# Kernel tuning notes

Measured on AMD Instinct MI355X. Metric: run time of the kernel, lower is better.

## Reference

```python
import math
import jax, jax.numpy as jnp
import numpy as np

DIM = 192
HEADS = 4
OUT_DIM = 192

def _conv(x, w, groups=1, pad=0):
    return jax.lax.conv_general_dilated(
        x, w, window_strides=(1, 1), padding=[(pad, pad), (pad, pad)],
        feature_group_count=groups, dimension_numbers=('NCHW', 'OIHW', 'NCHW'))

def setup_inputs() -> dict:
    key = jax.random.key(0)
    ks = jax.random.split(key, 8)
    b, c, h, w = 8, DIM, 128, 128
    x = jax.random.normal(ks[0], (b, c, h, w), dtype=jnp.float32)
    y = jax.random.normal(ks[1], (b, c, h, w), dtype=jnp.float32)
    s = 0.02
    kv_w = jax.random.normal(ks[2], (2 * DIM, DIM, 1, 1), dtype=jnp.float32) * s
    kv_dw_w = jax.random.normal(ks[3], (2 * DIM, 1, 3, 3), dtype=jnp.float32) * s  # depthwise, groups=2*dim
    q_w = jax.random.normal(ks[4], (DIM, DIM, 1, 1), dtype=jnp.float32) * s
    q_dw_w = jax.random.normal(ks[5], (DIM, DIM, 3, 3), dtype=jnp.float32) * s  # dense 3x3 (groups=1 in source)
    proj_w = jax.random.normal(ks[6], (OUT_DIM, DIM, 1, 1), dtype=jnp.float32) * s
    temperature = jnp.ones((HEADS, 1, 1), dtype=jnp.float32)
    return {"x": x, "y": y, "kv_w": kv_w, "kv_dw_w": kv_dw_w, "q_w": q_w,
            "q_dw_w": q_dw_w, "proj_w": proj_w, "temperature": temperature}

def _l2norm(t, eps=1e-12):
    # matches torch F.normalize(dim=-1)
    n = jnp.sqrt(jnp.sum(t * t, axis=-1, keepdims=True))
    return t / jnp.maximum(n, eps)

def reference(x, y, kv_w, kv_dw_w, q_w, q_dw_w, proj_w, temperature):
    b, c, h, w = x.shape
    hw = h * w
    ch = c // HEADS  # channels per head
    kv = _conv(_conv(x, kv_w), kv_dw_w, groups=2 * c, pad=1)  # [b, 2c, h, w]
    k, v = jnp.split(kv, 2, axis=1)
    q = _conv(_conv(y, q_w), q_dw_w, pad=1)  # [b, c, h, w]
    # b (head ch) h w -> b head ch (h w)
    q = q.reshape(b, HEADS, ch, hw)
    k = k.reshape(b, HEADS, ch, hw)
    v = v.reshape(b, HEADS, ch, hw)
    q = _l2norm(q)
    k = _l2norm(k)
    attn = jnp.einsum('bhcn,bhdn->bhcd', q, k)  # channel-wise attention [b,H,ch,ch]
    temp = temperature * math.log(attn.shape[-1])  # [H,1,1]
    attn = jax.nn.softmax(attn * temp[None], axis=-1)
    out = jnp.einsum('bhcd,bhdn->bhcn', attn, v)  # [b,H,ch,hw]
    out = out.reshape(b, c, h, w)
    return _conv(out, proj_w)
```

## Files before the change

### kernel.cpp

```cpp
#include <hip/hip_runtime.h>


#define HW 16384

using f32x4  = __attribute__((ext_vector_type(4))) float;
using bf16x8 = __attribute__((ext_vector_type(8))) __bf16;
using u16x8  = __attribute__((ext_vector_type(8))) unsigned short;
typedef unsigned short u16;

__device__ __forceinline__ u16 f2bf(float f) {
  unsigned u = __builtin_bit_cast(unsigned, f);
  u = (u + 0x7fffu + ((u >> 16) & 1u)) >> 16;
  return (u16)u;
}
__device__ __forceinline__ float bf2f(u16 s) {
  unsigned u = ((unsigned)s) << 16;
  return __builtin_bit_cast(float, u);
}

__device__ __forceinline__ void g2l16(const void* g, void* l) {
  __builtin_amdgcn_global_load_lds(
      (const __attribute__((address_space(1))) unsigned int*)g,
      (__attribute__((address_space(3))) unsigned int*)l, 16, 0, 0);
}

__global__ __launch_bounds__(256) void pack_w1(
    const float* __restrict__ kv_w, u16* __restrict__ W1) {
  int i = blockIdx.x * 256 + threadIdx.x;
  W1[i] = f2bf(kv_w[i]);
}

__global__ __launch_bounds__(192) void make_w4(
    const float* __restrict__ q_w, const float* __restrict__ q_dw_w,
    u16* __restrict__ W4) {
  const int o = blockIdx.x / 9, seg = blockIdx.x % 9;
  const int c = threadIdx.x;
  float s = 0.f;
  for (int ic = 0; ic < 192; ++ic)
    s += q_dw_w[(o * 192 + ic) * 9 + seg] * q_w[ic * 192 + c];
  W4[o * 1728 + seg * 192 + c] = f2bf(s);
}

template <typename TIn>
__global__ __launch_bounds__(256) void transpose_kernel(
    const TIn* __restrict__ src, u16* __restrict__ dst, int srcCstride) {
  __shared__ u16 tile[32][34];
  const int bz = blockIdx.z;
  const int n0 = blockIdx.x * 32;
  const int c0 = blockIdx.y * 32;
  const TIn* s = src + (long)bz * srcCstride * HW;
  u16* d = dst + (long)bz * HW * 192;
  const int tx = threadIdx.x & 31;
  const int ty = threadIdx.x >> 5;
#pragma unroll
  for (int i = 0; i < 32; i += 8) {
    if constexpr (sizeof(TIn) == 4)
      tile[ty + i][tx] = f2bf(((const float*)s)[(long)(c0 + ty + i) * HW + n0 + tx]);
    else
      tile[ty + i][tx] = ((const u16*)s)[(long)(c0 + ty + i) * HW + n0 + tx];
  }
  __syncthreads();
#pragma unroll
  for (int i = 0; i < 32; i += 8)
    d[(long)(n0 + ty + i) * 192 + c0 + tx] = tile[tx][ty + i];
}

template <int NSEG, bool OUT_BF16, bool FUSE_RQ>
__global__ __launch_bounds__(256, 3) void gemm_kernel(
    const u16* __restrict__ A, const u16* __restrict__ Bt,
    void* __restrict__ Cout, const u16* __restrict__ zp,
    int M, long aBatchStride, float* __restrict__ rqs) {
  __shared__ __align__(16) u16 shA[4096];
  __shared__ __align__(16) u16 shB[16384];
  const int Ktot = NSEG * 192;
  const int tid = threadIdx.x;
  const int w = tid >> 6;
  const int lane = tid & 63;
  const int rl = lane & 15;
  const int q4 = lane >> 4;
  const int wm = w & 1, wn = w >> 1;
  const int b = blockIdx.z;
  const int n0 = blockIdx.x * 256;
  const int m0 = blockIdx.y * 64;

  const u16* Ab = A + (long)b * aBatchStride + (long)m0 * Ktot;
  const u16* Btb = Bt + (long)b * HW * 192;
  const char* asrc = (const char*)(Ab + (long)(w * 16 + rl) * Ktot) + q4 * 16;

  f32x4 acc[2][8];
#pragma unroll
  for (int i = 0; i < 2; ++i)
#pragma unroll
    for (int j = 0; j < 8; ++j) acc[i][j] = f32x4{0.f, 0.f, 0.f, 0.f};

  const int lane_off = lane * 8;

  for (int seg = 0; seg < NSEG; ++seg) {
    const char* bsrc[4];
    if constexpr (NSEG == 1) {
#pragma unroll
      for (int j = 0; j < 4; ++j) {
        int n = n0 + (w * 4 + j) * 16 + rl;
        bsrc[j] = (const char*)(Btb + (long)n * 192) + q4 * 16;
      }
    } else {
      int dy = seg / 3 - 1, dx = seg % 3 - 1;
#pragma unroll
      for (int j = 0; j < 4; ++j) {
        int n = n0 + (w * 4 + j) * 16 + rl;
        int xx = n & 127, yy = n >> 7;
        bool ok = ((unsigned)(xx + dx) < 128u) && ((unsigned)(yy + dy) < 128u);
        bsrc[j] = ok ? (const char*)(Btb + (long)(n + dy * 128 + dx) * 192) + q4 * 16
                     : (const char*)zp + q4 * 16;
      }
    }
    const long acol = (long)seg * 192;
#pragma unroll
    for (int kk = 0; kk < 192; kk += 64) {
      const long ao = (acol + kk) * 2;
      g2l16(asrc + ao, &shA[w * 1024]);
      g2l16(asrc + ao + 64, &shA[w * 1024 + 512]);
#pragma unroll
      for (int j = 0; j < 4; ++j) {
        g2l16(bsrc[j] + kk * 2, &shB[(w * 4 + j) * 1024]);
        g2l16(bsrc[j] + kk * 2 + 64, &shB[(w * 4 + j) * 1024 + 512]);
      }
      __syncthreads();
      bf16x8 af[2][2];
#pragma unroll
      for (int i = 0; i < 2; ++i)
#pragma unroll
        for (int h = 0; h < 2; ++h)
          af[i][h] = *(const bf16x8*)&shA[(wm * 2 + i) * 1024 + h * 512 + lane_off];
#pragma unroll
      for (int jh = 0; jh < 2; ++jh) {
        bf16x8 bfr[4][2];
#pragma unroll
        for (int j2 = 0; j2 < 4; ++j2)
#pragma unroll
          for (int h = 0; h < 2; ++h)
            bfr[j2][h] = *(const bf16x8*)&shB[(wn * 8 + jh * 4 + j2) * 1024 + h * 512 + lane_off];
#pragma unroll
        for (int i = 0; i < 2; ++i)
#pragma unroll
          for (int j2 = 0; j2 < 4; ++j2) {
            const int j = jh * 4 + j2;
            acc[i][j] = __builtin_amdgcn_mfma_f32_16x16x32_bf16(af[i][0], bfr[j2][0], acc[i][j], 0, 0, 0);
            acc[i][j] = __builtin_amdgcn_mfma_f32_16x16x32_bf16(af[i][1], bfr[j2][1], acc[i][j], 0, 0, 0);
          }
      }
      __syncthreads();
    }
  }
  const int mb = m0 + wm * 32;
  const int nb = n0 + wn * 128;
  if constexpr (OUT_BF16) {
    u16* Cb = (u16*)Cout + (long)b * M * HW;
#pragma unroll
    for (int i = 0; i < 2; ++i)
#pragma unroll
      for (int j = 0; j < 8; ++j)
#pragma unroll
        for (int r = 0; r < 4; ++r)
          Cb[(long)(mb + i * 16 + q4 * 4 + r) * HW + nb + j * 16 + rl] = f2bf(acc[i][j][r]);
  } else {
    float* Cb = (float*)Cout + (long)b * M * HW;
#pragma unroll
    for (int i = 0; i < 2; ++i)
#pragma unroll
      for (int j = 0; j < 8; ++j)
#pragma unroll
        for (int r = 0; r < 4; ++r)
          Cb[(long)(mb + i * 16 + q4 * 4 + r) * HW + nb + j * 16 + rl] = acc[i][j][r];
  }
  if constexpr (FUSE_RQ) {
#pragma unroll
    for (int i = 0; i < 2; ++i)
#pragma unroll
      for (int r = 0; r < 4; ++r) {
        float s = 0.f;
#pragma unroll
        for (int j = 0; j < 8; ++j) s += acc[i][j][r] * acc[i][j][r];
        s += __shfl_xor(s, 1, 64);
        s += __shfl_xor(s, 2, 64);
        s += __shfl_xor(s, 4, 64);
        s += __shfl_xor(s, 8, 64);
        if (rl == 0)
          atomicAdd(&rqs[b * 192 + mb + i * 16 + q4 * 4 + r], s);
      }
  }
}

template <bool FUSE_NORM>
__global__ __launch_bounds__(256) void dwconv_kernel(
    const u16* __restrict__ kv, const float* __restrict__ dww,
    u16* __restrict__ dst, int cbase, int dstCstride, float* __restrict__ rks) {
  __shared__ __align__(16) u16 sp[HW];
  const int c = blockIdx.x;
  const int b = blockIdx.y;
  const int c2 = cbase + c;
  const u16* src = kv + ((long)b * 384 + c2) * HW;
  u16* out = dst + ((long)b * dstCstride + c) * HW;
  const int tid = threadIdx.x;
#pragma unroll
  for (int it = 0; it < 8; ++it)
    ((u16x8*)sp)[it * 256 + tid] = ((const u16x8*)src)[it * 256 + tid];
  __syncthreads();
  float w9[9];
#pragma unroll
  for (int t = 0; t < 9; ++t) w9[t] = dww[c2 * 9 + t];
  float ssum = 0.f;
  for (int o = 0; o < 8; ++o) {
    const int base = o * 2048 + tid * 8;
    const int yy = base >> 7;
    const int x0 = base & 127;
    float vv[3][10];
#pragma unroll
    for (int r = 0; r < 3; ++r) {
      int yr = yy + r - 1;
      if (yr >= 0 && yr < 128) {
        const u16* rp = sp + yr * 128 + x0;
        u16x8 mid = *(const u16x8*)rp;
#pragma unroll
        for (int i2 = 0; i2 < 8; ++i2) vv[r][1 + i2] = bf2f(mid[i2]);
        vv[r][0] = (x0 > 0)   ? bf2f(rp[-1]) : 0.f;
        vv[r][9] = (x0 < 120) ? bf2f(rp[8])  : 0.f;
      } else {
#pragma unroll
        for (int i2 = 0; i2 < 10; ++i2) vv[r][i2] = 0.f;
      }
    }
    u16x8 ov;
#pragma unroll
    for (int i2 = 0; i2 < 8; ++i2) {
      float s = 0.f;
#pragma unroll
      for (int r = 0; r < 3; ++r)
#pragma unroll
        for (int d = 0; d < 3; ++d) s += w9[r * 3 + d] * vv[r][i2 + d];
      if constexpr (FUSE_NORM) ssum += s * s;
      ov[i2] = f2bf(s);
    }
    *(u16x8*)(out + base) = ov;
  }
  if constexpr (FUSE_NORM) {
#pragma unroll
    for (int off = 32; off; off >>= 1) ssum += __shfl_down(ssum, off, 64);
    if ((tid & 63) == 0) atomicAdd(&rks[b * 192 + c], ssum);
  }
}

__global__ __launch_bounds__(256) void gram_kernel(
    const u16* __restrict__ qq, const u16* __restrict__ kk, float* __restrict__ gram) {
  __shared__ float red[4 * 2304];
  const int bh = blockIdx.x;
  const int kc = blockIdx.y;
  const int b = bh >> 2, h = bh & 3;
  const u16* qb = qq + ((long)b * 192 + h * 48) * HW;
  const u16* kb = kk + ((long)b * 192 + h * 48) * HW;
  const int tid = threadIdx.x, w = tid >> 6, lane = tid & 63;
  const int rl = lane & 15, q4 = lane >> 4;
  f32x4 acc[3][3];
#pragma unroll
  for (int i = 0; i < 3; ++i)
#pragma unroll
    for (int j = 0; j < 3; ++j) acc[i][j] = f32x4{0.f, 0.f, 0.f, 0.f};
  for (int tt = 0; tt < 16; ++tt) {
    const int k0 = ((kc * 16 + tt) * 4 + w) * 32 + q4 * 8;
    bf16x8 af[3], bfr[3];
#pragma unroll
    for (int i = 0; i < 3; ++i) af[i] = *(const bf16x8*)(qb + (long)(i * 16 + rl) * HW + k0);
#pragma unroll
    for (int j = 0; j < 3; ++j) bfr[j] = *(const bf16x8*)(kb + (long)(j * 16 + rl) * HW + k0);
#pragma unroll
    for (int i = 0; i < 3; ++i)
#pragma unroll
      for (int j = 0; j < 3; ++j)
        acc[i][j] = __builtin_amdgcn_mfma_f32_16x16x32_bf16(af[i], bfr[j], acc[i][j], 0, 0, 0);
  }
#pragma unroll
  for (int i = 0; i < 3; ++i)
#pragma unroll
    for (int j = 0; j < 3; ++j)
#pragma unroll
      for (int r = 0; r < 4; ++r)
        red[w * 2304 + (i * 16 + q4 * 4 + r) * 48 + j * 16 + rl] = acc[i][j][r];
  __syncthreads();
  for (int e = tid; e < 2304; e += 256)
    atomicAdd(&gram[(long)bh * 2304 + e], red[e] + red[2304 + e] + red[4608 + e] + red[6912 + e]);
}

__global__ __launch_bounds__(64) void softmax_kernel(
    const float* __restrict__ gram, const float* __restrict__ rqs,
    const float* __restrict__ rks, const float* __restrict__ temperature,
    float* __restrict__ attn) {
  const int R = blockIdx.x;
  const int lane = threadIdx.x;
  const int b = R / 192;
  const int h = (R % 192) / 48;
  const float ts = temperature[h] * 3.8712010109078907f;
  const float rq = rsqrtf(fmaxf(rqs[R], 1e-24f));
  float val = -3.0e38f;
  if (lane < 48) {
    const float rk = rsqrtf(fmaxf(rks[b * 192 + h * 48 + lane], 1e-24f));
    val = gram[(long)R * 48 + lane] * rq * rk * ts;
  }
  float mx = val;
#pragma unroll
  for (int off = 32; off; off >>= 1) mx = fmaxf(mx, __shfl_xor(mx, off, 64));
  float ex = (lane < 48) ? expf(val - mx) : 0.f;
  float sm = ex;
#pragma unroll
  for (int off = 32; off; off >>= 1) sm += __shfl_xor(sm, off, 64);
  if (lane < 48) attn[(long)R * 48 + lane] = ex / sm;
}

__global__ __launch_bounds__(192) void pa_kernel(
    const float* __restrict__ proj_w, const float* __restrict__ attn,
    u16* __restrict__ PA) {
  const int b = blockIdx.x;
  const int o = blockIdx.y;
  const int dg = threadIdx.x;
  const int hg = dg / 48, dl = dg % 48;
  const float* arow = attn + ((long)(b * 4 + hg) * 48) * 48 + dl;
  const float* prow = proj_w + o * 192 + hg * 48;
  float s = 0.f;
#pragma unroll
  for (int cl = 0; cl < 48; ++cl) s += prow[cl] * arow[(long)cl * 48];
  PA[((long)b * 192 + o) * 192 + dg] = f2bf(s);
}

extern "C" void kernel_launch(void* const* d_in, const int* in_sizes, int n_in,
                              void* d_out, int out_size, void* d_ws, size_t ws_size,
                              hipStream_t stream) {
  (void)in_sizes; (void)n_in; (void)out_size; (void)ws_size;
  const float* x        = (const float*)d_in[0];
  const float* y        = (const float*)d_in[1];
  const float* kv_w     = (const float*)d_in[2];
  const float* kv_dw_w  = (const float*)d_in[3];
  const float* q_w      = (const float*)d_in[4];
  const float* q_dw_w   = (const float*)d_in[5];
  const float* proj_w   = (const float*)d_in[6];
  const float* temperature = (const float*)d_in[7];

  char* ws = (char*)d_ws;
  u16* KV = (u16*)(ws + 0L);
  u16* R0 = (u16*)(ws + 100663296L);
  u16* R1 = (u16*)(ws + 150994944L);
  u16* R2 = (u16*)(ws + 201326592L);
  char* tail = ws + 251658240L;
  u16*   zp   = (u16*)(tail + 0);
  float* rqs  = (float*)(tail + 512);
  float* rks  = (float*)(tail + 6656);
  float* gram = (float*)(tail + 12800);
  float* attn = (float*)(tail + 307712);
  u16*   W1   = (u16*)(tail + 602624);
  u16*   W4   = (u16*)(tail + 750080);
  u16*   PA   = (u16*)(tail + 1413632);

  hipMemsetAsync(tail, 0, 307712, stream);
  pack_w1<<<288, 256, 0, stream>>>(kv_w, W1);
  make_w4<<<1728, 192, 0, stream>>>(q_w, q_dw_w, W4);

  transpose_kernel<float><<<dim3(512, 6, 8), 256, 0, stream>>>(y, R2, 192);
  gemm_kernel<9, true, true><<<dim3(64, 3, 8), 256, 0, stream>>>(W4, R2, R1, zp, 192, 0, rqs);

  transpose_kernel<float><<<dim3(512, 6, 8), 256, 0, stream>>>(x, R2, 192);
  gemm_kernel<1, true, false><<<dim3(64, 6, 8), 256, 0, stream>>>(W1, R2, KV, zp, 384, 0, nullptr);
  dwconv_kernel<true><<<dim3(192, 8), 256, 0, stream>>>(KV, kv_dw_w, R0, 0, 192, rks);
  dwconv_kernel<false><<<dim3(192, 8), 256, 0, stream>>>(KV, kv_dw_w, KV, 192, 384, nullptr);
  transpose_kernel<u16><<<dim3(512, 6, 8), 256, 0, stream>>>(KV, R2, 384);

  gram_kernel<<<dim3(32, 8), 256, 0, stream>>>(R1, R0, gram);
  softmax_kernel<<<1536, 64, 0, stream>>>(gram, rqs, rks, temperature, attn);
  pa_kernel<<<dim3(8, 192), 192, 0, stream>>>(proj_w, attn, PA);
  gemm_kernel<1, false, false><<<dim3(64, 3, 8), 256, 0, stream>>>(PA, R2, d_out, zp, 192, 36864, nullptr);
}
```

Before: 671.8 us.

## Double-buffer LDS tiles in GEMM to overlap global loads with MFMA

```diff
diff --git a/kernel.cpp b/kernel.cpp
--- a/kernel.cpp
+++ b/kernel.cpp
@@ -66,13 +66,14 @@
 }
 
 template <int NSEG, bool OUT_BF16, bool FUSE_RQ>
-__global__ __launch_bounds__(256, 3) void gemm_kernel(
+__global__ __launch_bounds__(256, 2) void gemm_kernel(
     const u16* __restrict__ A, const u16* __restrict__ Bt,
     void* __restrict__ Cout, const u16* __restrict__ zp,
     int M, long aBatchStride, float* __restrict__ rqs) {
-  __shared__ __align__(16) u16 shA[4096];
-  __shared__ __align__(16) u16 shB[16384];
+  __shared__ __align__(16) u16 shA[2][4096];
+  __shared__ __align__(16) u16 shB[2][16384];
   const int Ktot = NSEG * 192;
+  const int NT = NSEG * 3;
   const int tid = threadIdx.x;
   const int w = tid >> 6;
   const int lane = tid & 63;
@@ -86,6 +87,17 @@
   const u16* Ab = A + (long)b * aBatchStride + (long)m0 * Ktot;
   const u16* Btb = Bt + (long)b * HW * 192;
   const char* asrc = (const char*)(Ab + (long)(w * 16 + rl) * Ktot) + q4 * 16;
+  const char* zpp = (const char*)zp + q4 * 16;
+
+  const char* p0[4];
+  int xx[4], yy[4];
+#pragma unroll
+  for (int j = 0; j < 4; ++j) {
+    int n = n0 + (w * 4 + j) * 16 + rl;
+    p0[j] = (const char*)(Btb + (long)n * 192) + q4 * 16;
+    xx[j] = n & 127;
+    yy[j] = n >> 7;
+  }
 
   f32x4 acc[2][8];
 #pragma unroll
@@ -95,63 +107,71 @@
 
   const int lane_off = lane * 8;
 
-  for (int seg = 0; seg < NSEG; ++seg) {
-    const char* bsrc[4];
+  auto stage = [&](int t, int sbuf) {
+    const long ao = (long)t * 128;
+    g2l16(asrc + ao, &shA[sbuf][w * 1024]);
+    g2l16(asrc + ao + 64, &shA[sbuf][w * 1024 + 512]);
+    const char* bp[4];
+    int kb;
     if constexpr (NSEG == 1) {
+      kb = t * 128;
+#pragma unroll
+      for (int j = 0; j < 4; ++j) bp[j] = p0[j];
+    } else {
+      const int seg = t / 3;
+      kb = (t - seg * 3) * 128;
+      const int dy = seg / 3 - 1, dx = seg % 3 - 1;
+      const int roff = (dy * 128 + dx) * 384;
 #pragma unroll
       for (int j = 0; j < 4; ++j) {
-        int n = n0 + (w * 4 + j) * 16 + rl;
-        bsrc[j] = (const char*)(Btb + (long)n * 192) + q4 * 16;
+        bool ok = ((unsigned)(xx[j] + dx) < 128u) && ((unsigned)(yy[j] + dy) < 128u);
+        bp[j] = ok ? p0[j] + roff : zpp;
       }
-    } else {
-      int dy = seg / 3 - 1, dx = seg % 3 - 1;
-#pragma unroll
-      for (int j = 0; j < 4; ++j) {
-        int n = n0 + (w * 4 + j) * 16 + rl;
-        int xx = n & 127, yy = n >> 7;
-        bool ok = ((unsigned)(xx + dx) < 128u) && ((unsigned)(yy + dy) < 128u);
-        bsrc[j] = ok ? (const char*)(Btb + (long)(n + dy * 128 + dx) * 192) + q4 * 16
-                     : (const char*)zp + q4 * 16;
-      }
-    }
-    const long acol = (long)seg * 192;
-#pragma unroll
-    for (int kk = 0; kk < 192; kk += 64) {
-      const long ao = (acol + kk) * 2;
-      g2l16(asrc + ao, &shA[w * 1024]);
-      g2l16(asrc + ao + 64, &shA[w * 1024 + 512]);
-#pragma unroll
-      for (int j = 0; j < 4; ++j) {
-        g2l16(bsrc[j] + kk * 2, &shB[(w * 4 + j) * 1024]);
-        g2l16(bsrc[j] + kk * 2 + 64, &shB[(w * 4 + j) * 1024 + 512]);
-      }
-      __syncthreads();
-      bf16x8 af[2][2];
+    }
+#pragma unroll
+    for (int j = 0; j < 4; ++j) {
+      g2l16(bp[j] + kb, &shB[sbuf][(w * 4 + j) * 1024]);
+      g2l16(bp[j] + kb + 64, &shB[sbuf][(w * 4 + j) * 1024 + 512]);
+    }
+  };
+
+  auto compute = [&](int cbuf) {
+    bf16x8 af[2][2];
+#pragma unroll
+    for (int i = 0; i < 2; ++i)
+#pragma unroll
+      for (int h = 0; h < 2; ++h)
+        af[i][h] = *(const bf16x8*)&shA[cbuf][(wm * 2 + i) * 1024 + h * 512 + lane_off];
+#pragma unroll
+    for (int jh = 0; jh < 2; ++jh) {
+      bf16x8 bfr[4][2];
+#pragma unroll
+      for (int j2 = 0; j2 < 4; ++j2)
+#pragma unroll
+        for (int h = 0; h < 2; ++h)
+          bfr[j2][h] = *(const bf16x8*)&shB[cbuf][(wn * 8 + jh * 4 + j2) * 1024 + h * 512 + lane_off];
 #pragma unroll
       for (int i = 0; i < 2; ++i)
 #pragma unroll
-        for (int h = 0; h < 2; ++h)
-          af[i][h] = *(const bf16x8*)&shA[(wm * 2 + i) * 1024 + h * 512 + lane_off];
-#pragma unroll
-      for (int jh = 0; jh < 2; ++jh) {
-        bf16x8 bfr[4][2];
-#pragma unroll
-        for (int j2 = 0; j2 < 4; ++j2)
-#pragma unroll
-          for (int h = 0; h < 2; ++h)
-            bfr[j2][h] = *(const bf16x8*)&shB[(wn * 8 + jh * 4 + j2) * 1024 + h * 512 + lane_off];
-#pragma unroll
-        for (int i = 0; i < 2; ++i)
-#pragma unroll
-          for (int j2 = 0; j2 < 4; ++j2) {
-            const int j = jh * 4 + j2;
-            acc[i][j] = __builtin_amdgcn_mfma_f32_16x16x32_bf16(af[i][0], bfr[j2][0], acc[i][j], 0, 0, 0);
-            acc[i][j] = __builtin_amdgcn_mfma_f32_16x16x32_bf16(af[i][1], bfr[j2][1], acc[i][j], 0, 0, 0);
-          }
-      }
-      __syncthreads();
-    }
-  }
+        for (int j2 = 0; j2 < 4; ++j2) {
+          const int j = jh * 4 + j2;
+          acc[i][j] = __builtin_amdgcn_mfma_f32_16x16x32_bf16(af[i][0], bfr[j2][0], acc[i][j], 0, 0, 0);
+          acc[i][j] = __builtin_amdgcn_mfma_f32_16x16x32_bf16(af[i][1], bfr[j2][1], acc[i][j], 0, 0, 0);
+        }
+    }
+  };
+
+  stage(0, 0);
+  __syncthreads();
+  int cur = 0;
+  for (int t = 0; t < NT - 1; ++t) {
+    stage(t + 1, cur ^ 1);
+    compute(cur);
+    __syncthreads();
+    cur ^= 1;
+  }
+  compute(cur);
+
   const int mb = m0 + wm * 32;
   const int nb = n0 + wn * 128;
   if constexpr (OUT_BF16) {
```

Result: no change. 681.3 us (+1.4%).
